# Kernel tuning notes

Measured on AMD Instinct MI355X. Metric: run time of the kernel, lower is better.

## Reference

```python
import jax, jax.numpy as jnp
import numpy as np


def _conv(x, w, b, stride, pad):
    # x: [N,C,H,W], w: [O,I,kh,kw]
    y = jax.lax.conv_general_dilated(
        x, w, (stride, stride), [(pad, pad), (pad, pad)],
        dimension_numbers=('NCHW', 'OIHW', 'NCHW'))
    return y + b[None, :, None, None]


def _block(x, w1, b1, w2, b2, stride):
    # BasicBlock with BN folded: conv3x3 -> relu -> conv3x3
    h = jax.nn.relu(_conv(x, w1, b1, stride, 1))
    return _conv(h, w2, b2, 1, 1)


def setup_inputs() -> dict:
    key = jax.random.key(0)
    keys = iter(jax.random.split(key, 64))

    def rn(shape):
        fan_in = int(np.prod(shape[1:])) if len(shape) > 1 else shape[0]
        return jax.random.normal(next(keys), shape, jnp.float32) * (1.0 / np.sqrt(fan_in))

    d = {}
    d['inputs'] = jax.random.normal(next(keys), (128, 3, 64, 64), jnp.float32)
    d['probs'] = jax.random.uniform(next(keys), (128, 15), jnp.float32)
    d['seed_w'] = rn((64, 3, 3, 3))
    d['seed_b'] = jnp.zeros((64,), jnp.float32)
    specs = [(64, 64), (64, 128), (128, 256)]  # (cin, cout) per group
    for g, (ci, co) in enumerate(specs):
        d[f'g{g}_ds_w'] = rn((co, ci, 1, 1))
        d[f'g{g}_ds_b'] = jnp.zeros((co,), jnp.float32)
        d[f'g{g}_b0_w1'] = rn((co, ci, 3, 3))
        d[f'g{g}_b0_b1'] = jnp.zeros((co,), jnp.float32)
        d[f'g{g}_b0_w2'] = rn((co, co, 3, 3))
        d[f'g{g}_b0_b2'] = jnp.zeros((co,), jnp.float32)
        d[f'g{g}_r_w1'] = rn((4, co, co, 3, 3))
        d[f'g{g}_r_b1'] = jnp.zeros((4, co), jnp.float32)
        d[f'g{g}_r_w2'] = rn((4, co, co, 3, 3))
        d[f'g{g}_r_b2'] = jnp.zeros((4, co), jnp.float32)
    d['fc_w'] = rn((1000, 256))
    d['fc_b'] = jnp.zeros((1000,), jnp.float32)
    return d


def reference(inputs, probs, seed_w, seed_b,
              g0_ds_w, g0_ds_b, g0_b0_w1, g0_b0_b1, g0_b0_w2, g0_b0_b2,
              g0_r_w1, g0_r_b1, g0_r_w2, g0_r_b2,
              g1_ds_w, g1_ds_b, g1_b0_w1, g1_b0_b1, g1_b0_w2, g1_b0_b2,
              g1_r_w1, g1_r_b1, g1_r_w2, g1_r_b2,
              g2_ds_w, g2_ds_b, g2_b0_w1, g2_b0_b1, g2_b0_w2, g2_b0_b2,
              g2_r_w1, g2_r_b1, g2_r_w2, g2_r_b2,
              fc_w, fc_b):
    # policy[k, n] in {0,1}: hard-threshold of agent probs at 0.5 (forward_real)
    policy = jnp.where(probs < 0.5, 0.0, 1.0).astype(inputs.dtype).T  # [15, B]
    x = jax.nn.relu(_conv(inputs, seed_w, seed_b, 1, 1))
    groups = [
        (g0_ds_w, g0_ds_b, g0_b0_w1, g0_b0_b1, g0_b0_w2, g0_b0_b2, g0_r_w1, g0_r_b1, g0_r_w2, g0_r_b2, 1),
        (g1_ds_w, g1_ds_b, g1_b0_w1, g1_b0_b1, g1_b0_w2, g1_b0_b2, g1_r_w1, g1_r_b1, g1_r_w2, g1_r_b2, 2),
        (g2_ds_w, g2_ds_b, g2_b0_w1, g2_b0_b1, g2_b0_w2, g2_b0_b2, g2_r_w1, g2_r_b1, g2_r_w2, g2_r_b2, 2),
    ]
    idx = 0
    for (ds_w, ds_b, b0_w1, b0_b1, b0_w2, b0_b2, r_w1, r_b1, r_w2, r_b2, s) in groups:
        # first block of the group: strided, with 1x1 downsample residual
        residual = _conv(x, ds_w, ds_b, s, 0)
        fx = _block(x, b0_w1, b0_b1, b0_w2, b0_b2, s)
        m = policy[idx][:, None, None, None]
        idx += 1
        x = m * jax.nn.relu(residual + fx) + (1.0 - m) * residual
        # remaining 4 identity-residual blocks
        for j in range(4):
            residual = x
            fx = _block(x, r_w1[j], r_b1[j], r_w2[j], r_b2[j], 1)
            m = policy[idx][:, None, None, None]
            idx += 1
            x = m * jax.nn.relu(residual + fx) + (1.0 - m) * residual
    pooled = x.mean(axis=(2, 3))  # global average pool [B, 256]
    return pooled @ fc_w.T + fc_b
```

## Files before the change

kernel.cpp:

```cpp
#include <hip/hip_runtime.h>

using bf = unsigned short;
typedef __attribute__((ext_vector_type(8))) short short8v;
typedef __attribute__((ext_vector_type(4))) float f32x4;
typedef __attribute__((ext_vector_type(4))) unsigned int u32x4;
typedef __attribute__((ext_vector_type(2))) unsigned int u32x2;

__device__ __forceinline__ float bf2f(bf u) { return __uint_as_float(((unsigned)u) << 16); }
__device__ __forceinline__ bf f2bf(float f) {
    unsigned x = __float_as_uint(f);
    x += 0x7fffu + ((x >> 16) & 1u);
    return (bf)(x >> 16);
}

__device__ __forceinline__ void gload16(const bf* g, bf* l) {
    __builtin_amdgcn_global_load_lds(
        (const __attribute__((address_space(1))) void*)g,
        (__attribute__((address_space(3))) void*)l, 16, 0, 0);
}

template <int CI, int CC, int RS, int STRIDE, bool RELU, bool COMBINE, int LOG2W>
__global__ __launch_bounds__(256) void conv_mfma(
    const bf* __restrict__ X, const bf* __restrict__ Wp,
    const float* __restrict__ bias, bf* __restrict__ Y,
    const bf* __restrict__ res, const float* __restrict__ probs,
    const bf* __restrict__ zpage, int kidx, int Co) {
    constexpr int W = 1 << LOG2W;
    constexpr int ROWS = 128 >> LOG2W;
    constexpr int PAD = (RS == 3) ? 1 : 0;
    constexpr int IN_ROWS = (ROWS - 1) * STRIDE + RS;
    constexpr int IN_COLS = (W - 1) * STRIDE + RS;
    constexpr int NG = CC / 8;
    constexpr int HIN = W * STRIDE;
    constexpr int RSRS = RS * RS;
    constexpr int NCH = CI / CC;
    constexpr bool DIRECT = (RS == 1);
    constexpr int TG = IN_ROWS * IN_COLS * NG;
    constexpr int NITER = (TG + 255) / 256;

    __shared__ bf sX[DIRECT ? 8 : IN_ROWS * IN_COLS * CC];

    const int tid = threadIdx.x;
    const int n = blockIdx.z;
    const int coBase = blockIdx.y << 6;
    const int r0 = blockIdx.x * ROWS;
    const size_t pixBase = (size_t)n * W * W + (size_t)r0 * W;

    bool active = true;
    if (kidx >= 0) active = (probs[n * 15 + kidx] >= 0.5f);
    if (!active) {
        if constexpr (COMBINE) {
            for (int i = tid; i < (128 * 64) / 8; i += 256) {
                size_t off = (pixBase + (i >> 3)) * Co + coBase + (i & 7) * 8;
                u32x4 v = *reinterpret_cast<const u32x4*>(res + off);
                *reinterpret_cast<u32x4*>(Y + off) = v;
            }
        }
        return;
    }

    const int lane = tid & 63;
    const int wid = tid >> 6;
    const int l15 = lane & 15;
    const int lq = lane >> 4;
    const int wm = wid >> 1;
    const int wn = wid & 1;

    f32x4 acc[2][4] = {};
    int prow[4], pcol[4];
#pragma unroll
    for (int nf = 0; nf < 4; ++nf) {
        int p = wn * 64 + nf * 16 + l15;
        prow[nf] = p >> LOG2W;
        pcol[nf] = p & (W - 1);
    }

    const bf* Xn = X + (size_t)n * HIN * HIN * CI;

    if constexpr (DIRECT) {
#pragma unroll
        for (int ch = 0; ch < NCH; ++ch) {
#pragma unroll
            for (int kk = 0; kk < CC / 32; ++kk) {
                short8v a[2], b[4];
#pragma unroll
                for (int mf = 0; mf < 2; ++mf) {
                    int co = coBase + wm * 32 + mf * 16 + l15;
                    a[mf] = *reinterpret_cast<const short8v*>(
                        Wp + ((size_t)ch * Co + co) * CC + kk * 32 + lq * 8);
                }
#pragma unroll
                for (int nf = 0; nf < 4; ++nf) {
                    b[nf] = *reinterpret_cast<const short8v*>(
                        Xn + ((size_t)((r0 + prow[nf]) * STRIDE) * HIN + pcol[nf] * STRIDE) * CI +
                        ch * CC + kk * 32 + lq * 8);
                }
#pragma unroll
                for (int mf = 0; mf < 2; ++mf)
#pragma unroll
                    for (int nf = 0; nf < 4; ++nf)
                        acc[mf][nf] = __builtin_amdgcn_mfma_f32_16x16x32_bf16(
                            a[mf], b[nf], acc[mf][nf], 0, 0, 0);
            }
        }
    } else {
        for (int ch = 0; ch < NCH; ++ch) {
            if (ch) __syncthreads();
#pragma unroll
            for (int i = 0; i < NITER; ++i) {
                int g = tid + i * 256;
                if (TG % 256 == 0 || g < TG) {
                    int ir = g / (IN_COLS * NG);
                    int rem = g - ir * (IN_COLS * NG);
                    int ic = rem / NG;
                    int gc = rem - ic * NG;
                    int in_r = r0 * STRIDE - PAD + ir;
                    int in_c = ic - PAD;
                    int gsrc = gc ^ (ic & (NG - 1));
                    const bf* src = zpage;
                    if ((unsigned)in_r < (unsigned)HIN && (unsigned)in_c < (unsigned)HIN)
                        src = Xn + ((size_t)in_r * HIN + in_c) * CI + ch * CC + gsrc * 8;
                    gload16(src, &sX[(size_t)g * 8]);
                }
            }
            __syncthreads();

            if constexpr (CC >= 32) {
#pragma unroll
                for (int j = 0; j < RSRS; ++j) {
                    const int dh = j / RS;
                    const int dw = j % RS;
#pragma unroll
                    for (int kk = 0; kk < CC / 32; ++kk) {
                        short8v a[2], b[4];
#pragma unroll
                        for (int mf = 0; mf < 2; ++mf) {
                            int co = coBase + wm * 32 + mf * 16 + l15;
                            a[mf] = *reinterpret_cast<const short8v*>(
                                Wp + (((size_t)(ch * RSRS + j) * Co + co) * CC + kk * 32 + lq * 8));
                        }
#pragma unroll
                        for (int nf = 0; nf < 4; ++nf) {
                            int ir = prow[nf] * STRIDE + dh;
                            int ic = pcol[nf] * STRIDE + dw;
                            int gk = (kk * 4 + lq) ^ (ic & (NG - 1));
                            b[nf] = *reinterpret_cast<const short8v*>(
                                &sX[((ir * IN_COLS + ic) * NG + gk) * 8]);
                        }
#pragma unroll
                        for (int mf = 0; mf < 2; ++mf)
#pragma unroll
                            for (int nf = 0; nf < 4; ++nf)
                                acc[mf][nf] = __builtin_amdgcn_mfma_f32_16x16x32_bf16(
                                    a[mf], b[nf], acc[mf][nf], 0, 0, 0);
                    }
                }
            } else {
#pragma unroll
                for (int kt = 0; kt < 3; ++kt) {
                    int j = kt * 4 + lq;
                    int jj = (j < 9) ? j : 0;
                    int dh = jj / 3, dw = jj % 3;
                    short8v a[2], b[4];
#pragma unroll
                    for (int mf = 0; mf < 2; ++mf) {
                        int co = coBase + wm * 32 + mf * 16 + l15;
                        a[mf] = *reinterpret_cast<const short8v*>(Wp + ((size_t)j * Co + co) * 8);
                    }
#pragma unroll
                    for (int nf = 0; nf < 4; ++nf) {
                        int ir = prow[nf] + dh;
                        int ic = pcol[nf] + dw;
                        b[nf] = *reinterpret_cast<const short8v*>(&sX[(ir * IN_COLS + ic) * 8]);
                    }
#pragma unroll
                    for (int mf = 0; mf < 2; ++mf)
#pragma unroll
                        for (int nf = 0; nf < 4; ++nf)
                            acc[mf][nf] = __builtin_amdgcn_mfma_f32_16x16x32_bf16(
                                a[mf], b[nf], acc[mf][nf], 0, 0, 0);
                }
            }
        }
    }

#pragma unroll
    for (int mf = 0; mf < 2; ++mf) {
        int co0 = coBase + wm * 32 + mf * 16 + lq * 4;
        float4 b4 = *reinterpret_cast<const float4*>(bias + co0);
        float bb[4] = {b4.x, b4.y, b4.z, b4.w};
#pragma unroll
        for (int nf = 0; nf < 4; ++nf) {
            int p = wn * 64 + nf * 16 + l15;
            size_t off = (pixBase + p) * Co + co0;
            float v[4];
#pragma unroll
            for (int i = 0; i < 4; ++i) v[i] = acc[mf][nf][i] + bb[i];
            if constexpr (COMBINE) {
                u32x2 r2 = *reinterpret_cast<const u32x2*>(res + off);
                bf rr[4] = {(bf)(r2[0] & 0xffff), (bf)(r2[0] >> 16),
                            (bf)(r2[1] & 0xffff), (bf)(r2[1] >> 16)};
#pragma unroll
                for (int i = 0; i < 4; ++i) v[i] = fmaxf(v[i] + bf2f(rr[i]), 0.f);
            }
            if constexpr (RELU) {
#pragma unroll
                for (int i = 0; i < 4; ++i) v[i] = fmaxf(v[i], 0.f);
            }
            unsigned lo = (unsigned)f2bf(v[0]) | ((unsigned)f2bf(v[1]) << 16);
            unsigned hi = (unsigned)f2bf(v[2]) | ((unsigned)f2bf(v[3]) << 16);
            u32x2 o2 = {lo, hi};
            *reinterpret_cast<u32x2*>(Y + off) = o2;
        }
    }
}

#define NSEG 34
struct Seg {
    const float* src;
    bf* dst;
    int Co, Ci, RSRS, CC, JPAD, blk0;
};
struct SegArgs {
    Seg s[NSEG];
};
__global__ void repack_all(SegArgs A) {
    int b = blockIdx.x;
    int lo = 0;
#pragma unroll 1
    for (int i = 1; i < NSEG; ++i)
        if (A.s[i].blk0 <= b) lo = i;
    Seg sg = A.s[lo];
    int NCH_ = (sg.Ci + sg.CC - 1) / sg.CC;
    size_t total = (size_t)NCH_ * sg.JPAD * sg.Co * sg.CC;
    size_t idx = (size_t)(b - sg.blk0) * 256 + threadIdx.x;
    if (idx >= total) return;
    int cw = (int)(idx % sg.CC);
    int co = (int)((idx / sg.CC) % sg.Co);
    int j = (int)((idx / ((size_t)sg.CC * sg.Co)) % sg.JPAD);
    int ch = (int)(idx / ((size_t)sg.CC * sg.Co * sg.JPAD));
    int ci = ch * sg.CC + cw;
    float v = 0.f;
    if (ci < sg.Ci && j < sg.RSRS) v = sg.src[((size_t)co * sg.Ci + ci) * sg.RSRS + j];
    sg.dst[idx] = f2bf(v);
}

__global__ void cvt_in(const float* __restrict__ in, bf* __restrict__ out) {
    size_t idx = (size_t)blockIdx.x * 256 + threadIdx.x;
    int c = (int)(idx & 7);
    size_t pix = idx >> 3;
    int w = (int)(pix & 63);
    int h = (int)((pix >> 6) & 63);
    int n = (int)(pix >> 12);
    float v = 0.f;
    if (c < 3) v = in[(((size_t)n * 3 + c) * 64 + h) * 64 + w];
    out[idx] = f2bf(v);
}

__global__ void zero_k(bf* p) {
    u32x4 z = {0, 0, 0, 0};
    *reinterpret_cast<u32x4*>(p + (size_t)threadIdx.x * 8) = z;
}

__global__ void pool_k(const bf* __restrict__ X, float* __restrict__ pooled) {
    __shared__ float red[8][256];
    int n = blockIdx.x;
    int g = threadIdx.x & 31;
    int slice = threadIdx.x >> 5;
    float acc[8] = {};
    for (int p = slice * 32; p < slice * 32 + 32; ++p) {
        u32x4 v = *reinterpret_cast<const u32x4*>(X + ((size_t)n * 256 + p) * 256 + g * 8);
#pragma unroll
        for (int i = 0; i < 4; ++i) {
            acc[2 * i] += bf2f((bf)(v[i] & 0xffff));
            acc[2 * i + 1] += bf2f((bf)(v[i] >> 16));
        }
    }
#pragma unroll
    for (int i = 0; i < 8; ++i) red[slice][g * 8 + i] = acc[i];
    __syncthreads();
    if (slice == 0) {
#pragma unroll
        for (int i = 0; i < 8; ++i) {
            float s = 0.f;
#pragma unroll
            for (int ss = 0; ss < 8; ++ss) s += red[ss][g * 8 + i];
            pooled[n * 256 + g * 8 + i] = s * (1.f / 256.f);
        }
    }
}

__global__ void fc_k(const float* __restrict__ pooled, const float* __restrict__ fw,
                     const float* __restrict__ fb, float* __restrict__ out) {
    __shared__ float sp[256];
    int n = blockIdx.x;
    sp[threadIdx.x] = pooled[n * 256 + threadIdx.x];
    __syncthreads();
    for (int o = threadIdx.x; o < 1000; o += 256) {
        float acc = fb[o];
        for (int k = 0; k < 256; ++k) acc += sp[k] * fw[(size_t)o * 256 + k];
        out[(size_t)n * 1000 + o] = acc;
    }
}

template <int CIN, int COUT, int S, int LW, int CC1>
static void run_group(hipStream_t st, bf* X, bf* H, bf* OUT, const bf* zp,
                      bf* wp_ds, const float* ds_b, bf* wp_w1, const float* b1,
                      bf* wp_w2, const float* b2, bf* const* wp_rw1, const float* rb1,
                      bf* const* wp_rw2, const float* rb2, const float* probs_c,
                      int kbase, int NB) {
    constexpr int Wo = 1 << LW;
    dim3 grid((Wo * Wo) / 128, COUT / 64, NB);
    conv_mfma<CIN, 64, 1, S, false, false, LW><<<grid, 256, 0, st>>>(
        X, wp_ds, ds_b, OUT, nullptr, nullptr, zp, -1, COUT);
    conv_mfma<CIN, CC1, 3, S, true, false, LW><<<grid, 256, 0, st>>>(
        X, wp_w1, b1, H, nullptr, probs_c, zp, kbase, COUT);
    conv_mfma<COUT, 64, 3, 1, false, true, LW><<<grid, 256, 0, st>>>(
        H, wp_w2, b2, OUT, OUT, probs_c, zp, kbase, COUT);
    for (int j = 0; j < 4; ++j) {
        conv_mfma<COUT, 64, 3, 1, true, false, LW><<<grid, 256, 0, st>>>(
            OUT, wp_rw1[j], rb1 + j * COUT, H, nullptr, probs_c, zp, kbase + 1 + j, COUT);
        conv_mfma<COUT, 64, 3, 1, false, true, LW><<<grid, 256, 0, st>>>(
            H, wp_rw2[j], rb2 + j * COUT, OUT, OUT, probs_c, zp, kbase + 1 + j, COUT);
    }
}

extern "C" void kernel_launch(void* const* d_in, const int* in_sizes, int n_in,
                              void* d_out, int out_size, void* d_ws, size_t ws_size,
                              hipStream_t stream) {
    (void)in_sizes; (void)n_in; (void)out_size;
    const float* input = (const float*)d_in[0];
    const float* probs = (const float*)d_in[1];
    const float* seed_w = (const float*)d_in[2];
    const float* seed_b = (const float*)d_in[3];
    const float* fc_w = (const float*)d_in[34];
    const float* fc_b = (const float*)d_in[35];

    char* pw = (char*)d_ws;
    auto alloc = [&](size_t bytes) -> void* {
        void* r = (void*)pw;
        pw += ((bytes + 255) & ~(size_t)255);
        return r;
    };

    bf* xin = (bf*)alloc(128ull * 64 * 64 * 8 * 2);
    float* pooled = (float*)alloc(128 * 256 * 4);
    bf* zpage = (bf*)alloc(256);

    SegArgs sa;
    int nseg = 0;
    int blkAcc = 0;
    auto pack = [&](const float* w, int Co_, int Ci_, int RSRS_, int CC_, int JPAD_) -> bf* {
        int NCH_ = (Ci_ + CC_ - 1) / CC_;
        size_t total = (size_t)NCH_ * JPAD_ * Co_ * CC_;
        bf* wp = (bf*)alloc(total * 2);
        sa.s[nseg] = {w, wp, Co_, Ci_, RSRS_, CC_, JPAD_, blkAcc};
        blkAcc += (int)((total + 255) / 256);
        ++nseg;
        return wp;
    };

    zero_k<<<dim3(1), 16, 0, stream>>>(zpage);
    cvt_in<<<dim3(16384), 256, 0, stream>>>(input, xin);

    bf* wpSeed = pack(seed_w, 64, 3, 9, 8, 12);
    const int cis[3] = {64, 64, 128};
    const int cos[3] = {64, 128, 256};
    const int cc1s[3] = {64, 32, 32};
    bf* wp_ds[3];
    bf* wp_w1[3];
    bf* wp_w2[3];
    bf* wp_rw1[3][4];
    bf* wp_rw2[3][4];
    const float *ds_b[3], *b1[3], *b2[3], *rb1[3], *rb2[3];
    for (int g = 0; g < 3; ++g) {
        int base = 4 + g * 10;
        const float* dsw = (const float*)d_in[base + 0];
        ds_b[g] = (const float*)d_in[base + 1];
        const float* w1 = (const float*)d_in[base + 2];
        b1[g] = (const float*)d_in[base + 3];
        const float* w2 = (const float*)d_in[base + 4];
        b2[g] = (const float*)d_in[base + 5];
        const float* rw1 = (const float*)d_in[base + 6];
        rb1[g] = (const float*)d_in[base + 7];
        const float* rw2 = (const float*)d_in[base + 8];
        rb2[g] = (const float*)d_in[base + 9];
        int Ci = cis[g], Co = cos[g];
        wp_ds[g] = pack(dsw, Co, Ci, 1, 64, 1);
        wp_w1[g] = pack(w1, Co, Ci, 9, cc1s[g], 9);
        wp_w2[g] = pack(w2, Co, Co, 9, 64, 9);
        for (int j = 0; j < 4; ++j) {
            wp_rw1[g][j] = pack(rw1 + (size_t)j * Co * Co * 9, Co, Co, 9, 64, 9);
            wp_rw2[g][j] = pack(rw2 + (size_t)j * Co * Co * 9, Co, Co, 9, 64, 9);
        }
    }
    for (int i = nseg; i < NSEG; ++i) sa.s[i] = {nullptr, nullptr, 1, 1, 1, 1, 1, 0x7fffffff};
    repack_all<<<dim3(blkAcc), 256, 0, stream>>>(sa);

    size_t used = (size_t)(pw - (char*)d_ws);
    size_t avail = (ws_size > used) ? (ws_size - used) : 0;
    const size_t PER_IMG = 64ull * 64 * 64 * 2;
    int NB = 128;
    while (NB > 8 && (size_t)3 * NB * PER_IMG + 4096 > avail) NB >>= 1;

    bf* A = (bf*)alloc((size_t)NB * PER_IMG);
    bf* Bb = (bf*)alloc((size_t)NB * PER_IMG);
    bf* C = (bf*)alloc((size_t)NB * PER_IMG);

    for (int n0 = 0; n0 < 128; n0 += NB) {
        const float* pc = probs + (size_t)n0 * 15;
        conv_mfma<8, 8, 3, 1, true, false, 6><<<dim3(32, 1, NB), 256, 0, stream>>>(
            xin + (size_t)n0 * 64 * 64 * 8, wpSeed, seed_b, A, nullptr, nullptr, zpage, -1, 64);

        run_group<64, 64, 1, 6, 64>(stream, A, Bb, C, zpage, wp_ds[0], ds_b[0], wp_w1[0], b1[0],
                                    wp_w2[0], b2[0], wp_rw1[0], rb1[0], wp_rw2[0], rb2[0],
                                    pc, 0, NB);
        run_group<64, 128, 2, 5, 32>(stream, C, Bb, A, zpage, wp_ds[1], ds_b[1], wp_w1[1], b1[1],
                                     wp_w2[1], b2[1], wp_rw1[1], rb1[1], wp_rw2[1], rb2[1],
                                     pc, 5, NB);
        run_group<128, 256, 2, 4, 32>(stream, A, Bb, C, zpage, wp_ds[2], ds_b[2], wp_w1[2], b1[2],
                                      wp_w2[2], b2[2], wp_rw1[2], rb1[2], wp_rw2[2], rb2[2],
                                      pc, 10, NB);

        pool_k<<<dim3(NB), 256, 0, stream>>>(C, pooled + (size_t)n0 * 256);
    }

    fc_k<<<dim3(128), 256, 0, stream>>>(pooled, fc_w, fc_b, (float*)d_out);
}
```

Before: 2.040 ms.

## Double-buffer LDS input tiles across channel chunks and drop redundant inactive copies

For 3x3 convolutions with several input-channel chunks, the input tile is now staged into a second LDS buffer while the current chunk is computed, which removes one barrier per chunk and hides the global-to-LDS load latency. Skipped blocks no longer copy the residual into the output, because the combine kernels are launched with output and residual as the same buffer, so that copy did nothing. Launch bounds now request 3 blocks per CU. The larger LDS footprint and the occupancy hint could raise register pressure or limit how many blocks fit on a CU.

```diff
diff --git a/kernel.cpp b/kernel.cpp
--- a/kernel.cpp
+++ b/kernel.cpp
@@ -19,8 +19,8 @@
         (__attribute__((address_space(3))) void*)l, 16, 0, 0);
 }
 
-template <int CI, int CC, int RS, int STRIDE, bool RELU, bool COMBINE, int LOG2W>
-__global__ __launch_bounds__(256) void conv_mfma(
+template <int CI, int CC, int RS, int STRIDE, bool RELU, int CMB, int LOG2W>
+__global__ __launch_bounds__(256, 3) void conv_mfma(
     const bf* __restrict__ X, const bf* __restrict__ Wp,
     const float* __restrict__ bias, bf* __restrict__ Y,
     const bf* __restrict__ res, const float* __restrict__ probs,
@@ -37,8 +37,10 @@
     constexpr bool DIRECT = (RS == 1);
     constexpr int TG = IN_ROWS * IN_COLS * NG;
     constexpr int NITER = (TG + 255) / 256;
-
-    __shared__ bf sX[DIRECT ? 8 : IN_ROWS * IN_COLS * CC];
+    constexpr int HALF = IN_ROWS * IN_COLS * CC;
+    constexpr bool DBUF = (!DIRECT) && (NCH > 1) && (2 * HALF * 2 <= 65536);
+
+    __shared__ bf sX[DIRECT ? 8 : (DBUF ? 2 * HALF : HALF)];
 
     const int tid = threadIdx.x;
     const int n = blockIdx.z;
@@ -48,16 +50,7 @@
 
     bool active = true;
     if (kidx >= 0) active = (probs[n * 15 + kidx] >= 0.5f);
-    if (!active) {
-        if constexpr (COMBINE) {
-            for (int i = tid; i < (128 * 64) / 8; i += 256) {
-                size_t off = (pixBase + (i >> 3)) * Co + coBase + (i & 7) * 8;
-                u32x4 v = *reinterpret_cast<const u32x4*>(res + off);
-                *reinterpret_cast<u32x4*>(Y + off) = v;
-            }
-        }
-        return;
-    }
+    if (!active) return;
 
     const int lane = tid & 63;
     const int wid = tid >> 6;
@@ -104,8 +97,7 @@
             }
         }
     } else {
-        for (int ch = 0; ch < NCH; ++ch) {
-            if (ch) __syncthreads();
+        auto stage = [&](int ch, bf* buf) {
 #pragma unroll
             for (int i = 0; i < NITER; ++i) {
                 int g = tid + i * 256;
@@ -120,11 +112,12 @@
                     const bf* src = zpage;
                     if ((unsigned)in_r < (unsigned)HIN && (unsigned)in_c < (unsigned)HIN)
                         src = Xn + ((size_t)in_r * HIN + in_c) * CI + ch * CC + gsrc * 8;
-                    gload16(src, &sX[(size_t)g * 8]);
+                    gload16(src, &buf[(size_t)g * 8]);
                 }
             }
-            __syncthreads();
-
+        };
+
+        auto compute = [&](int ch, const bf* buf) {
             if constexpr (CC >= 32) {
 #pragma unroll
                 for (int j = 0; j < RSRS; ++j) {
@@ -145,7 +138,7 @@
                             int ic = pcol[nf] * STRIDE + dw;
                             int gk = (kk * 4 + lq) ^ (ic & (NG - 1));
                             b[nf] = *reinterpret_cast<const short8v*>(
-                                &sX[((ir * IN_COLS + ic) * NG + gk) * 8]);
+                                &buf[((ir * IN_COLS + ic) * NG + gk) * 8]);
                         }
 #pragma unroll
                         for (int mf = 0; mf < 2; ++mf)
@@ -171,7 +164,7 @@
                     for (int nf = 0; nf < 4; ++nf) {
                         int ir = prow[nf] + dh;
                         int ic = pcol[nf] + dw;
-                        b[nf] = *reinterpret_cast<const short8v*>(&sX[(ir * IN_COLS + ic) * 8]);
+                        b[nf] = *reinterpret_cast<const short8v*>(&buf[(ir * IN_COLS + ic) * 8]);
                     }
 #pragma unroll
                     for (int mf = 0; mf < 2; ++mf)
@@ -181,6 +174,26 @@
                                 a[mf], b[nf], acc[mf][nf], 0, 0, 0);
                 }
             }
+        };
+
+        if constexpr (DBUF) {
+            stage(0, sX);
+            __syncthreads();
+#pragma unroll
+            for (int ch = 0; ch < NCH; ++ch) {
+                bf* cur = sX + (size_t)(ch & 1) * HALF;
+                bf* nxt = sX + (size_t)((ch + 1) & 1) * HALF;
+                if (ch + 1 < NCH) stage(ch + 1, nxt);
+                compute(ch, cur);
+                if (ch + 1 < NCH) __syncthreads();
+            }
+        } else {
+            for (int ch = 0; ch < NCH; ++ch) {
+                if (ch) __syncthreads();
+                stage(ch, sX);
+                __syncthreads();
+                compute(ch, sX);
+            }
         }
     }
 
@@ -196,7 +209,7 @@
             float v[4];
 #pragma unroll
             for (int i = 0; i < 4; ++i) v[i] = acc[mf][nf][i] + bb[i];
-            if constexpr (COMBINE) {
+            if constexpr (CMB >= 1) {
                 u32x2 r2 = *reinterpret_cast<const u32x2*>(res + off);
                 bf rr[4] = {(bf)(r2[0] & 0xffff), (bf)(r2[0] >> 16),
                             (bf)(r2[1] & 0xffff), (bf)(r2[1] >> 16)};
@@ -311,16 +324,16 @@
                       int kbase, int NB) {
     constexpr int Wo = 1 << LW;
     dim3 grid((Wo * Wo) / 128, COUT / 64, NB);
-    conv_mfma<CIN, 64, 1, S, false, false, LW><<<grid, 256, 0, st>>>(
+    conv_mfma<CIN, 64, 1, S, false, 0, LW><<<grid, 256, 0, st>>>(
         X, wp_ds, ds_b, OUT, nullptr, nullptr, zp, -1, COUT);
-    conv_mfma<CIN, CC1, 3, S, true, false, LW><<<grid, 256, 0, st>>>(
+    conv_mfma<CIN, CC1, 3, S, true, 0, LW><<<grid, 256, 0, st>>>(
         X, wp_w1, b1, H, nullptr, probs_c, zp, kbase, COUT);
-    conv_mfma<COUT, 64, 3, 1, false, true, LW><<<grid, 256, 0, st>>>(
+    conv_mfma<COUT, 64, 3, 1, false, 2, LW><<<grid, 256, 0, st>>>(
         H, wp_w2, b2, OUT, OUT, probs_c, zp, kbase, COUT);
     for (int j = 0; j < 4; ++j) {
-        conv_mfma<COUT, 64, 3, 1, true, false, LW><<<grid, 256, 0, st>>>(
+        conv_mfma<COUT, 64, 3, 1, true, 0, LW><<<grid, 256, 0, st>>>(
             OUT, wp_rw1[j], rb1 + j * COUT, H, nullptr, probs_c, zp, kbase + 1 + j, COUT);
-        conv_mfma<COUT, 64, 3, 1, false, true, LW><<<grid, 256, 0, st>>>(
+        conv_mfma<COUT, 64, 3, 1, false, 2, LW><<<grid, 256, 0, st>>>(
             H, wp_rw2[j], rb2 + j * COUT, OUT, OUT, probs_c, zp, kbase + 1 + j, COUT);
     }
 }
@@ -409,7 +422,7 @@
 
     for (int n0 = 0; n0 < 128; n0 += NB) {
         const float* pc = probs + (size_t)n0 * 15;
-        conv_mfma<8, 8, 3, 1, true, false, 6><<<dim3(32, 1, NB), 256, 0, stream>>>(
+        conv_mfma<8, 8, 3, 1, true, 0, 6><<<dim3(32, 1, NB), 256, 0, stream>>>(
             xin + (size_t)n0 * 64 * 64 * 8, wpSeed, seed_b, A, nullptr, nullptr, zpage, -1, 64);
 
         run_group<64, 64, 1, 6, 64>(stream, A, Bb, C, zpage, wp_ds[0], ds_b[0], wp_w1[0], b1[0],
```

Result: no change. 2.020 ms (-1.0%).

## Use 2D spatial tiles in conv kernel, drop inactive copy, vectorize weight repack

Applied to the files above, without the earlier changes.

Replaces the full-row pixel tiling in the MFMA conv kernel with templated 2D tiles (TH x TW). This cuts the halo overhead for stride-2 and small feature maps. The last group uses 8x8 tiles, which gives each block fewer pixels but puts more blocks in flight. The LDS swizzle now uses ic>>1 for stride-2 loads, and launch bounds request 3 blocks per CU. Inactive blocks now return immediately instead of copying the residual, which is safe because output and residual are the same buffer. Weight repacking writes 8 bf16 values per thread with one vector store. Risks: smaller tiles lower per-block MFMA work and weight reuse, and the occupancy hint may force register spills.

```diff
diff --git a/kernel.cpp b/kernel.cpp
--- a/kernel.cpp
+++ b/kernel.cpp
@@ -19,17 +19,15 @@
         (__attribute__((address_space(3))) void*)l, 16, 0, 0);
 }
 
-template <int CI, int CC, int RS, int STRIDE, bool RELU, bool COMBINE, int LOG2W>
-__global__ __launch_bounds__(256) void conv_mfma(
+template <int CI, int CC, int RS, int STRIDE, bool RELU, int CMB, int TH, int TW, int W>
+__global__ __launch_bounds__(256, 3) void conv_mfma(
     const bf* __restrict__ X, const bf* __restrict__ Wp,
     const float* __restrict__ bias, bf* __restrict__ Y,
     const bf* __restrict__ res, const float* __restrict__ probs,
     const bf* __restrict__ zpage, int kidx, int Co) {
-    constexpr int W = 1 << LOG2W;
-    constexpr int ROWS = 128 >> LOG2W;
     constexpr int PAD = (RS == 3) ? 1 : 0;
-    constexpr int IN_ROWS = (ROWS - 1) * STRIDE + RS;
-    constexpr int IN_COLS = (W - 1) * STRIDE + RS;
+    constexpr int IN_ROWS = (TH - 1) * STRIDE + RS;
+    constexpr int IN_COLS = (TW - 1) * STRIDE + RS;
     constexpr int NG = CC / 8;
     constexpr int HIN = W * STRIDE;
     constexpr int RSRS = RS * RS;
@@ -37,27 +35,23 @@
     constexpr bool DIRECT = (RS == 1);
     constexpr int TG = IN_ROWS * IN_COLS * NG;
     constexpr int NITER = (TG + 255) / 256;
+    constexpr int NPX = TH * TW;
+    constexpr int NF = NPX / 32;
+    constexpr int TPR = W / TW;
+    constexpr int KSH = (STRIDE == 2) ? 1 : 0;
 
     __shared__ bf sX[DIRECT ? 8 : IN_ROWS * IN_COLS * CC];
 
     const int tid = threadIdx.x;
     const int n = blockIdx.z;
     const int coBase = blockIdx.y << 6;
-    const int r0 = blockIdx.x * ROWS;
-    const size_t pixBase = (size_t)n * W * W + (size_t)r0 * W;
+    const int bx = blockIdx.x;
+    const int tr0 = (bx / TPR) * TH;
+    const int tc0 = (bx % TPR) * TW;
 
     bool active = true;
     if (kidx >= 0) active = (probs[n * 15 + kidx] >= 0.5f);
-    if (!active) {
-        if constexpr (COMBINE) {
-            for (int i = tid; i < (128 * 64) / 8; i += 256) {
-                size_t off = (pixBase + (i >> 3)) * Co + coBase + (i & 7) * 8;
-                u32x4 v = *reinterpret_cast<const u32x4*>(res + off);
-                *reinterpret_cast<u32x4*>(Y + off) = v;
-            }
-        }
-        return;
-    }
+    if (!active) return;
 
     const int lane = tid & 63;
     const int wid = tid >> 6;
@@ -66,13 +60,13 @@
     const int wm = wid >> 1;
     const int wn = wid & 1;
 
-    f32x4 acc[2][4] = {};
-    int prow[4], pcol[4];
-#pragma unroll
-    for (int nf = 0; nf < 4; ++nf) {
-        int p = wn * 64 + nf * 16 + l15;
-        prow[nf] = p >> LOG2W;
-        pcol[nf] = p & (W - 1);
+    f32x4 acc[2][NF] = {};
+    int prow[NF], pcol[NF];
+#pragma unroll
+    for (int nf = 0; nf < NF; ++nf) {
+        int p = wn * (NPX / 2) + nf * 16 + l15;
+        prow[nf] = p / TW;
+        pcol[nf] = p % TW;
     }
 
     const bf* Xn = X + (size_t)n * HIN * HIN * CI;
@@ -82,7 +76,7 @@
         for (int ch = 0; ch < NCH; ++ch) {
 #pragma unroll
             for (int kk = 0; kk < CC / 32; ++kk) {
-                short8v a[2], b[4];
+                short8v a[2], b[NF];
 #pragma unroll
                 for (int mf = 0; mf < 2; ++mf) {
                     int co = coBase + wm * 32 + mf * 16 + l15;
@@ -90,15 +84,15 @@
                         Wp + ((size_t)ch * Co + co) * CC + kk * 32 + lq * 8);
                 }
 #pragma unroll
-                for (int nf = 0; nf < 4; ++nf) {
+                for (int nf = 0; nf < NF; ++nf) {
                     b[nf] = *reinterpret_cast<const short8v*>(
-                        Xn + ((size_t)((r0 + prow[nf]) * STRIDE) * HIN + pcol[nf] * STRIDE) * CI +
-                        ch * CC + kk * 32 + lq * 8);
+                        Xn + ((size_t)((tr0 + prow[nf]) * STRIDE) * HIN +
+                              (tc0 + pcol[nf]) * STRIDE) * CI + ch * CC + kk * 32 + lq * 8);
                 }
 #pragma unroll
                 for (int mf = 0; mf < 2; ++mf)
 #pragma unroll
-                    for (int nf = 0; nf < 4; ++nf)
+                    for (int nf = 0; nf < NF; ++nf)
                         acc[mf][nf] = __builtin_amdgcn_mfma_f32_16x16x32_bf16(
                             a[mf], b[nf], acc[mf][nf], 0, 0, 0);
             }
@@ -114,9 +108,9 @@
                     int rem = g - ir * (IN_COLS * NG);
                     int ic = rem / NG;
                     int gc = rem - ic * NG;
-                    int in_r = r0 * STRIDE - PAD + ir;
-                    int in_c = ic - PAD;
-                    int gsrc = gc ^ (ic & (NG - 1));
+                    int in_r = tr0 * STRIDE - PAD + ir;
+                    int in_c = tc0 * STRIDE - PAD + ic;
+                    int gsrc = gc ^ ((ic >> KSH) & (NG - 1));
                     const bf* src = zpage;
                     if ((unsigned)in_r < (unsigned)HIN && (unsigned)in_c < (unsigned)HIN)
                         src = Xn + ((size_t)in_r * HIN + in_c) * CI + ch * CC + gsrc * 8;
@@ -132,7 +126,7 @@
                     const int dw = j % RS;
 #pragma unroll
                     for (int kk = 0; kk < CC / 32; ++kk) {
-                        short8v a[2], b[4];
+                        short8v a[2], b[NF];
 #pragma unroll
                         for (int mf = 0; mf < 2; ++mf) {
                             int co = coBase + wm * 32 + mf * 16 + l15;
@@ -140,17 +134,17 @@
                                 Wp + (((size_t)(ch * RSRS + j) * Co + co) * CC + kk * 32 + lq * 8));
                         }
 #pragma unroll
-                        for (int nf = 0; nf < 4; ++nf) {
+                        for (int nf = 0; nf < NF; ++nf) {
                             int ir = prow[nf] * STRIDE + dh;
                             int ic = pcol[nf] * STRIDE + dw;
-                            int gk = (kk * 4 + lq) ^ (ic & (NG - 1));
+                            int gk = (kk * 4 + lq) ^ ((ic >> KSH) & (NG - 1));
                             b[nf] = *reinterpret_cast<const short8v*>(
                                 &sX[((ir * IN_COLS + ic) * NG + gk) * 8]);
                         }
 #pragma unroll
                         for (int mf = 0; mf < 2; ++mf)
 #pragma unroll
-                            for (int nf = 0; nf < 4; ++nf)
+                            for (int nf = 0; nf < NF; ++nf)
                                 acc[mf][nf] = __builtin_amdgcn_mfma_f32_16x16x32_bf16(
                                     a[mf], b[nf], acc[mf][nf], 0, 0, 0);
                     }
@@ -161,14 +155,14 @@
                     int j = kt * 4 + lq;
                     int jj = (j < 9) ? j : 0;
                     int dh = jj / 3, dw = jj % 3;
-                    short8v a[2], b[4];
+                    short8v a[2], b[NF];
 #pragma unroll
                     for (int mf = 0; mf < 2; ++mf) {
                         int co = coBase + wm * 32 + mf * 16 + l15;
                         a[mf] = *reinterpret_cast<const short8v*>(Wp + ((size_t)j * Co + co) * 8);
                     }
 #pragma unroll
-                    for (int nf = 0; nf < 4; ++nf) {
+                    for (int nf = 0; nf < NF; ++nf) {
                         int ir = prow[nf] + dh;
                         int ic = pcol[nf] + dw;
                         b[nf] = *reinterpret_cast<const short8v*>(&sX[(ir * IN_COLS + ic) * 8]);
@@ -176,7 +170,7 @@
 #pragma unroll
                     for (int mf = 0; mf < 2; ++mf)
 #pragma unroll
-                        for (int nf = 0; nf < 4; ++nf)
+                        for (int nf = 0; nf < NF; ++nf)
                             acc[mf][nf] = __builtin_amdgcn_mfma_f32_16x16x32_bf16(
                                 a[mf], b[nf], acc[mf][nf], 0, 0, 0);
                 }
@@ -190,13 +184,12 @@
         float4 b4 = *reinterpret_cast<const float4*>(bias + co0);
         float bb[4] = {b4.x, b4.y, b4.z, b4.w};
 #pragma unroll
-        for (int nf = 0; nf < 4; ++nf) {
-            int p = wn * 64 + nf * 16 + l15;
-            size_t off = (pixBase + p) * Co + co0;
+        for (int nf = 0; nf < NF; ++nf) {
+            size_t off = ((size_t)n * W * W + (size_t)(tr0 + prow[nf]) * W + tc0 + pcol[nf]) * Co + co0;
             float v[4];
 #pragma unroll
             for (int i = 0; i < 4; ++i) v[i] = acc[mf][nf][i] + bb[i];
-            if constexpr (COMBINE) {
+            if constexpr (CMB >= 1) {
                 u32x2 r2 = *reinterpret_cast<const u32x2*>(res + off);
                 bf rr[4] = {(bf)(r2[0] & 0xffff), (bf)(r2[0] >> 16),
                             (bf)(r2[1] & 0xffff), (bf)(r2[1] >> 16)};
@@ -232,17 +225,26 @@
         if (A.s[i].blk0 <= b) lo = i;
     Seg sg = A.s[lo];
     int NCH_ = (sg.Ci + sg.CC - 1) / sg.CC;
-    size_t total = (size_t)NCH_ * sg.JPAD * sg.Co * sg.CC;
-    size_t idx = (size_t)(b - sg.blk0) * 256 + threadIdx.x;
-    if (idx >= total) return;
-    int cw = (int)(idx % sg.CC);
-    int co = (int)((idx / sg.CC) % sg.Co);
-    int j = (int)((idx / ((size_t)sg.CC * sg.Co)) % sg.JPAD);
-    int ch = (int)(idx / ((size_t)sg.CC * sg.Co * sg.JPAD));
-    int ci = ch * sg.CC + cw;
-    float v = 0.f;
-    if (ci < sg.Ci && j < sg.RSRS) v = sg.src[((size_t)co * sg.Ci + ci) * sg.RSRS + j];
-    sg.dst[idx] = f2bf(v);
+    size_t total8 = ((size_t)NCH_ * sg.JPAD * sg.Co * sg.CC) >> 3;
+    size_t i8 = (size_t)(b - sg.blk0) * 256 + threadIdx.x;
+    if (i8 >= total8) return;
+    size_t e = i8 * 8;
+    int cw = (int)(e % sg.CC);
+    int co = (int)((e / sg.CC) % sg.Co);
+    int j = (int)((e / ((size_t)sg.CC * sg.Co)) % sg.JPAD);
+    int ch = (int)(e / ((size_t)sg.CC * sg.Co * sg.JPAD));
+    bf tmp[8];
+#pragma unroll
+    for (int k = 0; k < 8; ++k) {
+        int ci = ch * sg.CC + cw + k;
+        float v = 0.f;
+        if (ci < sg.Ci && j < sg.RSRS) v = sg.src[((size_t)co * sg.Ci + ci) * sg.RSRS + j];
+        tmp[k] = f2bf(v);
+    }
+    u32x4 o;
+#pragma unroll
+    for (int k = 0; k < 4; ++k) o[k] = (unsigned)tmp[2 * k] | ((unsigned)tmp[2 * k + 1] << 16);
+    *reinterpret_cast<u32x4*>(sg.dst + e) = o;
 }
 
 __global__ void cvt_in(const float* __restrict__ in, bf* __restrict__ out) {
@@ -303,24 +305,23 @@
     }
 }
 
-template <int CIN, int COUT, int S, int LW, int CC1>
+template <int CIN, int COUT, int S, int TH, int TW, int W, int CC1>
 static void run_group(hipStream_t st, bf* X, bf* H, bf* OUT, const bf* zp,
                       bf* wp_ds, const float* ds_b, bf* wp_w1, const float* b1,
                       bf* wp_w2, const float* b2, bf* const* wp_rw1, const float* rb1,
                       bf* const* wp_rw2, const float* rb2, const float* probs_c,
                       int kbase, int NB) {
-    constexpr int Wo = 1 << LW;
-    dim3 grid((Wo * Wo) / 128, COUT / 64, NB);
-    conv_mfma<CIN, 64, 1, S, false, false, LW><<<grid, 256, 0, st>>>(
+    dim3 grid((W / TH) * (W / TW), COUT / 64, NB);
+    conv_mfma<CIN, 64, 1, S, false, 0, TH, TW, W><<<grid, 256, 0, st>>>(
         X, wp_ds, ds_b, OUT, nullptr, nullptr, zp, -1, COUT);
-    conv_mfma<CIN, CC1, 3, S, true, false, LW><<<grid, 256, 0, st>>>(
+    conv_mfma<CIN, CC1, 3, S, true, 0, TH, TW, W><<<grid, 256, 0, st>>>(
         X, wp_w1, b1, H, nullptr, probs_c, zp, kbase, COUT);
-    conv_mfma<COUT, 64, 3, 1, false, true, LW><<<grid, 256, 0, st>>>(
+    conv_mfma<COUT, 64, 3, 1, false, 2, TH, TW, W><<<grid, 256, 0, st>>>(
         H, wp_w2, b2, OUT, OUT, probs_c, zp, kbase, COUT);
     for (int j = 0; j < 4; ++j) {
-        conv_mfma<COUT, 64, 3, 1, true, false, LW><<<grid, 256, 0, st>>>(
+        conv_mfma<COUT, 64, 3, 1, true, 0, TH, TW, W><<<grid, 256, 0, st>>>(
             OUT, wp_rw1[j], rb1 + j * COUT, H, nullptr, probs_c, zp, kbase + 1 + j, COUT);
-        conv_mfma<COUT, 64, 3, 1, false, true, LW><<<grid, 256, 0, st>>>(
+        conv_mfma<COUT, 64, 3, 1, false, 2, TH, TW, W><<<grid, 256, 0, st>>>(
             H, wp_rw2[j], rb2 + j * COUT, OUT, OUT, probs_c, zp, kbase + 1 + j, COUT);
     }
 }
@@ -355,7 +356,7 @@
         size_t total = (size_t)NCH_ * JPAD_ * Co_ * CC_;
         bf* wp = (bf*)alloc(total * 2);
         sa.s[nseg] = {w, wp, Co_, Ci_, RSRS_, CC_, JPAD_, blkAcc};
-        blkAcc += (int)((total + 255) / 256);
+        blkAcc += (int)(((total >> 3) + 255) / 256);
         ++nseg;
         return wp;
     };
@@ -409,18 +410,21 @@
 
     for (int n0 = 0; n0 < 128; n0 += NB) {
         const float* pc = probs + (size_t)n0 * 15;
-        conv_mfma<8, 8, 3, 1, true, false, 6><<<dim3(32, 1, NB), 256, 0, stream>>>(
+        conv_mfma<8, 8, 3, 1, true, 0, 8, 16, 64><<<dim3(32, 1, NB), 256, 0, stream>>>(
             xin + (size_t)n0 * 64 * 64 * 8, wpSeed, seed_b, A, nullptr, nullptr, zpage, -1, 64);
 
-        run_group<64, 64, 1, 6, 64>(stream, A, Bb, C, zpage, wp_ds[0], ds_b[0], wp_w1[0], b1[0],
-                                    wp_w2[0], b2[0], wp_rw1[0], rb1[0], wp_rw2[0], rb2[0],
-                                    pc, 0, NB);
-        run_group<64, 128, 2, 5, 32>(stream, C, Bb, A, zpage, wp_ds[1], ds_b[1], wp_w1[1], b1[1],
-                                     wp_w2[1], b2[1], wp_rw1[1], rb1[1], wp_rw2[1], rb2[1],
-                                     pc, 5, NB);
-        run_group<128, 256, 2, 4, 32>(stream, A, Bb, C, zpage, wp_ds[2], ds_b[2], wp_w1[2], b1[2],
-                                      wp_w2[2], b2[2], wp_rw1[2], rb1[2], wp_rw2[2], rb2[2],
-                                      pc, 10, NB);
+        run_group<64, 64, 1, 8, 16, 64, 64>(stream, A, Bb, C, zpage,
+                                            wp_ds[0], ds_b[0], wp_w1[0], b1[0],
+                                            wp_w2[0], b2[0], wp_rw1[0], rb1[0],
+                                            wp_rw2[0], rb2[0], pc, 0, NB);
+        run_group<64, 128, 2, 8, 16, 32, 32>(stream, C, Bb, A, zpage,
+                                             wp_ds[1], ds_b[1], wp_w1[1], b1[1],
+                                             wp_w2[1], b2[1], wp_rw1[1], rb1[1],
+                                             wp_rw2[1], rb2[1], pc, 5, NB);
+        run_group<128, 256, 2, 8, 8, 16, 32>(stream, A, Bb, C, zpage,
+                                             wp_ds[2], ds_b[2], wp_w1[2], b1[2],
+                                             wp_w2[2], b2[2], wp_rw1[2], rb1[2],
+                                             wp_rw2[2], rb2[2], pc, 10, NB);
 
         pool_k<<<dim3(NB), 256, 0, stream>>>(C, pooled + (size_t)n0 * 256);
     }
```

Result: slower. 2.360 ms (+15.7%).
